# Performance work log

Measured on AMD Instinct MI355X. Metric: run time of the kernel, lower is better.

Reference implementation:

```python
import jax, jax.numpy as jnp
import numpy as np

N_HEAD = 16
N_KV_HEAD = 4
HEAD_DIM = 128
EPS = 1e-6


def apply_rotary_emb(x, cos, sin):
    # x: (B,T,H,hd); cos/sin: (1,T,1,hd//2)
    d = x.shape[3] // 2
    x1, x2 = x[..., :d], x[..., d:]
    y1 = x1 * cos + x2 * sin
    y2 = x1 * -sin + x2 * cos
    return jnp.concatenate([y1, y2], axis=3).astype(x.dtype)


def rmsnorm(x):
    # flax nnx.RMSNorm with use_scale=False: x * rsqrt(mean(x^2) + eps)
    ms = jnp.mean(jnp.square(x), axis=-1, keepdims=True)
    return (x * jax.lax.rsqrt(ms + EPS)).astype(x.dtype)


def setup_inputs() -> dict:
    key = jax.random.key(0)
    ks = jax.random.split(key, 7)
    B, T, C = 4, 2048, 2048
    s = 0.02
    return {
        "x": jax.random.normal(ks[0], (B, T, C), jnp.float32),
        "cos": jax.random.normal(ks[1], (1, T, 1, HEAD_DIM // 2), jnp.float32),
        "sin": jax.random.normal(ks[2], (1, T, 1, HEAD_DIM // 2), jnp.float32),
        "Wq": jax.random.normal(ks[3], (C, N_HEAD * HEAD_DIM), jnp.float32) * s,
        "Wk": jax.random.normal(ks[4], (C, N_KV_HEAD * HEAD_DIM), jnp.float32) * s,
        "Wv": jax.random.normal(ks[5], (C, N_KV_HEAD * HEAD_DIM), jnp.float32) * s,
        "Wo": jax.random.normal(ks[6], (C, C), jnp.float32) * s,
    }


def reference(x, cos, sin, Wq, Wk, Wv, Wo):
    B, T, C = x.shape
    q = (x @ Wq).reshape(B, T, N_HEAD, HEAD_DIM)
    k = (x @ Wk).reshape(B, T, N_KV_HEAD, HEAD_DIM)
    v = (x @ Wv).reshape(B, T, N_KV_HEAD, HEAD_DIM)
    q = rmsnorm(apply_rotary_emb(q, cos, sin))
    k = rmsnorm(apply_rotary_emb(k, cos, sin))
    # (B,H,T,hd)
    q = jnp.transpose(q, (0, 2, 1, 3))
    k = jnp.transpose(k, (0, 2, 1, 3))
    v = jnp.transpose(v, (0, 2, 1, 3))
    nrep = N_HEAD // N_KV_HEAD
    k = jnp.repeat(k, nrep, axis=1)
    v = jnp.repeat(v, nrep, axis=1)
    scale = 1.0 / jnp.sqrt(jnp.float32(HEAD_DIM))
    att = jnp.einsum('bhqd,bhkd->bhqk', q, k) * scale
    mask = jnp.tril(jnp.ones((T, T), dtype=bool))[None, None, :, :]
    att = jnp.where(mask, att, -jnp.inf)
    att = jax.nn.softmax(att, axis=-1)
    y = jnp.einsum('bhqk,bhkd->bhqd', att, v)
    y = jnp.transpose(y, (0, 2, 1, 3)).reshape(B, T, -1)
    return y @ Wo
```

## Files before the change

kernel.cpp:

```cpp
#include <hip/hip_runtime.h>
#include <hip/hip_bf16.h>

typedef __attribute__((ext_vector_type(8))) short short8;
typedef __attribute__((ext_vector_type(4))) float f32x4;

#define B_SZ 4
#define T_SEQ 2048
#define C_DIM 2048
#define NH 16
#define NKV 4
#define HD 128

#define MFMA16 __builtin_amdgcn_mfma_f32_16x16x32_bf16

__device__ __forceinline__ unsigned short f2bf(float f) {
  union { __hip_bfloat16 h; unsigned short u; } v;
  v.h = __float2bfloat16(f);
  return v.u;
}
__device__ __forceinline__ float bf2f(unsigned short u) {
  union { unsigned short u; __hip_bfloat16 h; } v;
  v.u = u;
  return __bfloat162float(v.h);
}

__device__ __forceinline__ void gload_lds16(const unsigned short* g, unsigned short* l) {
  __builtin_amdgcn_global_load_lds(
      (const __attribute__((address_space(1))) unsigned int*)g,
      (__attribute__((address_space(3))) unsigned int*)l, 16, 0, 0);
}

__global__ void cast_x(const float* __restrict__ x, unsigned short* __restrict__ xb, int n4) {
  int i = blockIdx.x * blockDim.x + threadIdx.x;
  if (i < n4) {
    float4 f = ((const float4*)x)[i];
    ushort4 u = make_ushort4(f2bf(f.x), f2bf(f.y), f2bf(f.z), f2bf(f.w));
    ((ushort4*)xb)[i] = u;
  }
}

__global__ void wtransAll(const float* __restrict__ Wq, const float* __restrict__ Wk,
                          const float* __restrict__ Wv, const float* __restrict__ Wo,
                          unsigned short* __restrict__ WqkvT, unsigned short* __restrict__ WoT) {
  __shared__ float tile[32][33];
  int y = blockIdx.y;
  const float* W;
  unsigned short* Wt;
  int N, n0;
  if (y < 64) { W = Wq; Wt = WqkvT; N = 2048; n0 = y * 32; }
  else if (y < 80) { W = Wk; Wt = WqkvT + (size_t)2048 * 2048; N = 512; n0 = (y - 64) * 32; }
  else if (y < 96) { W = Wv; Wt = WqkvT + (size_t)2560 * 2048; N = 512; n0 = (y - 80) * 32; }
  else { W = Wo; Wt = WoT; N = 2048; n0 = (y - 96) * 32; }
  int k0 = blockIdx.x * 32;
  int tx = threadIdx.x, ty = threadIdx.y;
#pragma unroll
  for (int i = 0; i < 4; i++)
    tile[ty + i * 8][tx] = W[(size_t)(k0 + ty + i * 8) * N + n0 + tx];
  __syncthreads();
#pragma unroll
  for (int i = 0; i < 4; i++)
    Wt[(size_t)(n0 + ty + i * 8) * 2048 + k0 + tx] = f2bf(tile[tx][ty + i * 8]);
}

__global__ void vtrans(const unsigned short* __restrict__ qkv, unsigned short* __restrict__ Vt) {
  __shared__ unsigned short tile[32][34];
  int t0 = blockIdx.x * 32, d0 = blockIdx.y * 32;
  int b = blockIdx.z >> 2, kvh = blockIdx.z & 3;
  int tx = threadIdx.x, ty = threadIdx.y;
#pragma unroll
  for (int i = 0; i < 4; i++)
    tile[ty + i * 8][tx] =
        qkv[(size_t)(b * T_SEQ + t0 + ty + i * 8) * 3072 + 2560 + kvh * HD + d0 + tx];
  __syncthreads();
#pragma unroll
  for (int i = 0; i < 4; i++)
    Vt[((size_t)(b * NKV + kvh) * HD + d0 + ty + i * 8) * T_SEQ + t0 + tx] = tile[tx][ty + i * 8];
}

template <typename OutT>
__global__ __launch_bounds__(512, 2) void gemm128(const unsigned short* __restrict__ A,
                                                  const unsigned short* __restrict__ Bt,
                                                  OutT* __restrict__ Cc, int N, int K, int GX) {
  __shared__ alignas(16) unsigned short lds[2][3][128 * 64];
  const int tid = threadIdx.x, lane = tid & 63, wid = tid >> 6;
  const int wave_m = wid >> 2, wave_n = wid & 3;
  const int r16 = lane & 15, q4 = lane >> 4;
  const int sw = r16 & 7;

  int nwg = gridDim.x, orig = blockIdx.x;
  int qq = nwg >> 3, rr = nwg & 7;
  int xcd = orig & 7, loc = orig >> 3;
  int wg = (xcd < rr ? xcd * (qq + 1) : rr * (qq + 1) + (xcd - rr) * qq) + loc;
  int bx = wg % GX, by = wg / GX;
  const size_t row0 = (size_t)bx * 128, col0 = (size_t)by * 256;

  const unsigned short* Ab = A + row0 * K;
  const unsigned short* Bb0 = Bt + col0 * K;
  const unsigned short* Bb1 = Bt + (col0 + 128) * K;

  const int srow = lane >> 3, spb = lane & 7;
  auto stage = [&](const unsigned short* base, int buf, int slot, int k0) {
#pragma unroll
    for (int j = 0; j < 2; ++j) {
      int cw = j * 8 + wid;
      int row = cw * 8 + srow;
      gload_lds16(base + (size_t)row * K + k0 + ((spb ^ srow) * 8), &lds[buf][slot][cw * 512]);
    }
  };

  f32x4 acc[4][4];
  f32x4 zero = {0.f, 0.f, 0.f, 0.f};
#pragma unroll
  for (int m = 0; m < 4; m++)
#pragma unroll
    for (int n = 0; n < 4; n++) acc[m][n] = zero;

  const int NT = K / 64;
  stage(Ab, 0, 0, 0);
  stage(Bb0, 0, 1, 0);
  stage(Bb1, 0, 2, 0);
  stage(Ab, 1, 0, 64);
  asm volatile("s_waitcnt vmcnt(2)" ::: "memory");
  __builtin_amdgcn_s_barrier();

  short8 af[4][2], b01[2][2], b23[2][2];
  const int bslot = 1 + (wave_n >> 1);
  const int bro = (wave_n & 1) * 64;

  int cur = 0;
#pragma unroll 1
  for (int t = 0; t < NT; ++t) {
    const unsigned short* Ah = &lds[cur][0][0];
    const unsigned short* Bh = &lds[cur][bslot][0];
    const int k1 = t * 64 + 64, k2 = t * 64 + 128;
#pragma unroll
    for (int mf = 0; mf < 4; mf++)
#pragma unroll
      for (int kk = 0; kk < 2; kk++)
        af[mf][kk] =
            *(const short8*)(Ah + (wave_m * 64 + mf * 16 + r16) * 64 + (((kk * 4 + q4) ^ sw) * 8));
#pragma unroll
    for (int nf = 0; nf < 2; nf++)
#pragma unroll
      for (int kk = 0; kk < 2; kk++)
        b01[nf][kk] =
            *(const short8*)(Bh + (bro + nf * 16 + r16) * 64 + (((kk * 4 + q4) ^ sw) * 8));
    if (t + 1 < NT) stage(Bb0, cur ^ 1, 1, k1);
    __builtin_amdgcn_s_barrier();
    asm volatile("s_waitcnt lgkmcnt(0)" ::: "memory");
    __builtin_amdgcn_s_setprio(1);
#pragma unroll
    for (int mf = 0; mf < 4; mf++)
#pragma unroll
      for (int nf = 0; nf < 2; nf++)
#pragma unroll
        for (int kk = 0; kk < 2; kk++)
          acc[mf][nf] = MFMA16(af[mf][kk], b01[nf][kk], acc[mf][nf], 0, 0, 0);
    __builtin_amdgcn_s_setprio(0);
    __builtin_amdgcn_s_barrier();
#pragma unroll
    for (int nf = 0; nf < 2; nf++)
#pragma unroll
      for (int kk = 0; kk < 2; kk++)
        b23[nf][kk] =
            *(const short8*)(Bh + (bro + (nf + 2) * 16 + r16) * 64 + (((kk * 4 + q4) ^ sw) * 8));
    if (t + 1 < NT) stage(Bb1, cur ^ 1, 2, k1);
    if (t + 2 < NT) stage(Ab, cur, 0, k2);
    __builtin_amdgcn_s_barrier();
    asm volatile("s_waitcnt lgkmcnt(0)" ::: "memory");
    __builtin_amdgcn_s_setprio(1);
#pragma unroll
    for (int mf = 0; mf < 4; mf++)
#pragma unroll
      for (int nf = 0; nf < 2; nf++)
#pragma unroll
        for (int kk = 0; kk < 2; kk++)
          acc[mf][nf + 2] = MFMA16(af[mf][kk], b23[nf][kk], acc[mf][nf + 2], 0, 0, 0);
    __builtin_amdgcn_s_setprio(0);
    if (t + 2 < NT)
      asm volatile("s_waitcnt vmcnt(2)" ::: "memory");
    else if (t + 1 < NT)
      asm volatile("s_waitcnt vmcnt(0)" ::: "memory");
    __builtin_amdgcn_s_barrier();
    cur ^= 1;
  }

#pragma unroll
  for (int mf = 0; mf < 4; mf++)
#pragma unroll
    for (int nf = 0; nf < 4; nf++) {
      size_t rbase = row0 + wave_m * 64 + mf * 16 + q4 * 4;
      size_t cc = col0 + wave_n * 64 + nf * 16 + r16;
#pragma unroll
      for (int jj = 0; jj < 4; jj++) {
        if constexpr (sizeof(OutT) == 2)
          Cc[(rbase + jj) * (size_t)N + cc] = f2bf(acc[mf][nf][jj]);
        else
          Cc[(rbase + jj) * (size_t)N + cc] = acc[mf][nf][jj];
      }
    }
}

template <typename OutT>
__global__ __launch_bounds__(512, 2) void gemm256(const unsigned short* __restrict__ A,
                                                  const unsigned short* __restrict__ Bt,
                                                  OutT* __restrict__ Cc, int N, int K, int GX) {
  __shared__ alignas(16) unsigned short lds[2][4][128 * 64];
  const int tid = threadIdx.x, lane = tid & 63, wid = tid >> 6;
  const int wave_m = wid >> 2, wave_n = wid & 3;
  const int r16 = lane & 15, q4 = lane >> 4;
  const int sw = r16 & 7;

  int nwg = gridDim.x, orig = blockIdx.x;
  int qq = nwg >> 3, rr = nwg & 7;
  int xcd = orig & 7, loc = orig >> 3;
  int wg = (xcd < rr ? xcd * (qq + 1) : rr * (qq + 1) + (xcd - rr) * qq) + loc;
  int bx = wg % GX, by = wg / GX;
  const size_t row0 = (size_t)bx * 256, col0 = (size_t)by * 256;

  const unsigned short* Ab0 = A + row0 * K;
  const unsigned short* Ab1 = A + (row0 + 128) * K;
  const unsigned short* Bb0 = Bt + col0 * K;
  const unsigned short* Bb1 = Bt + (col0 + 128) * K;

  const int srow = lane >> 3, spb = lane & 7;
  auto stage = [&](const unsigned short* base, int buf, int slot, int k0) {
#pragma unroll
    for (int j = 0; j < 2; ++j) {
      int cw = j * 8 + wid;
      int row = cw * 8 + srow;
      gload_lds16(base + (size_t)row * K + k0 + ((spb ^ srow) * 8), &lds[buf][slot][cw * 512]);
    }
  };

  f32x4 acc[8][4];
  f32x4 zero = {0.f, 0.f, 0.f, 0.f};
#pragma unroll
  for (int m = 0; m < 8; m++)
#pragma unroll
    for (int n = 0; n < 4; n++) acc[m][n] = zero;

  const int NT = K / 64;
  stage(Ab0, 0, 0, 0);
  stage(Ab1, 0, 1, 0);
  stage(Bb0, 0, 2, 0);
  stage(Bb1, 0, 3, 0);
  stage(Ab0, 1, 0, 64);
  stage(Ab1, 1, 1, 64);
  asm volatile("s_waitcnt vmcnt(4)" ::: "memory");
  __builtin_amdgcn_s_barrier();

  short8 af[4][2], b01[2][2], b23[2][2];
  const int bslot = 2 + (wave_n >> 1);
  const int bro = (wave_n & 1) * 64;

  int cur = 0;
#pragma unroll 1
  for (int t = 0; t < NT; ++t) {
    const unsigned short* Ah = &lds[cur][wave_m][0];
    const unsigned short* Bh = &lds[cur][bslot][0];
    const int k1 = t * 64 + 64, k2 = t * 64 + 128;
#pragma unroll
    for (int mf = 0; mf < 4; mf++)
#pragma unroll
      for (int kk = 0; kk < 2; kk++)
        af[mf][kk] = *(const short8*)(Ah + (mf * 16 + r16) * 64 + (((kk * 4 + q4) ^ sw) * 8));
#pragma unroll
    for (int nf = 0; nf < 2; nf++)
#pragma unroll
      for (int kk = 0; kk < 2; kk++)
        b01[nf][kk] =
            *(const short8*)(Bh + (bro + nf * 16 + r16) * 64 + (((kk * 4 + q4) ^ sw) * 8));
    if (t + 1 < NT) stage(Bb0, cur ^ 1, 2, k1);
    __builtin_amdgcn_s_barrier();
    asm volatile("s_waitcnt lgkmcnt(0)" ::: "memory");
    __builtin_amdgcn_s_setprio(1);
#pragma unroll
    for (int mf = 0; mf < 4; mf++)
#pragma unroll
      for (int nf = 0; nf < 2; nf++)
#pragma unroll
        for (int kk = 0; kk < 2; kk++)
          acc[mf][nf] = MFMA16(af[mf][kk], b01[nf][kk], acc[mf][nf], 0, 0, 0);
    __builtin_amdgcn_s_setprio(0);
    __builtin_amdgcn_s_barrier();
#pragma unroll
    for (int nf = 0; nf < 2; nf++)
#pragma unroll
      for (int kk = 0; kk < 2; kk++)
        b23[nf][kk] =
            *(const short8*)(Bh + (bro + (nf + 2) * 16 + r16) * 64 + (((kk * 4 + q4) ^ sw) * 8));
    if (t + 1 < NT) stage(Bb1, cur ^ 1, 3, k1);
    __builtin_amdgcn_s_barrier();
    asm volatile("s_waitcnt lgkmcnt(0)" ::: "memory");
    __builtin_amdgcn_s_setprio(1);
#pragma unroll
    for (int mf = 0; mf < 4; mf++)
#pragma unroll
      for (int nf = 0; nf < 2; nf++)
#pragma unroll
        for (int kk = 0; kk < 2; kk++)
          acc[mf][nf + 2] = MFMA16(af[mf][kk], b23[nf][kk], acc[mf][nf + 2], 0, 0, 0);
    __builtin_amdgcn_s_setprio(0);
    __builtin_amdgcn_s_barrier();
#pragma unroll
    for (int mf = 0; mf < 4; mf++)
#pragma unroll
      for (int kk = 0; kk < 2; kk++)
        af[mf][kk] =
            *(const short8*)(Ah + ((mf + 4) * 16 + r16) * 64 + (((kk * 4 + q4) ^ sw) * 8));
    __builtin_amdgcn_s_barrier();
    asm volatile("s_waitcnt lgkmcnt(0)" ::: "memory");
    __builtin_amdgcn_s_setprio(1);
#pragma unroll
    for (int mf = 0; mf < 4; mf++)
#pragma unroll
      for (int nf = 0; nf < 2; nf++)
#pragma unroll
        for (int kk = 0; kk < 2; kk++)
          acc[mf + 4][nf] = MFMA16(af[mf][kk], b01[nf][kk], acc[mf + 4][nf], 0, 0, 0);
    __builtin_amdgcn_s_setprio(0);
    __builtin_amdgcn_s_barrier();
    if (t + 2 < NT) {
      stage(Ab0, cur, 0, k2);
      stage(Ab1, cur, 1, k2);
    }
    __builtin_amdgcn_s_barrier();
    __builtin_amdgcn_s_setprio(1);
#pragma unroll
    for (int mf = 0; mf < 4; mf++)
#pragma unroll
      for (int nf = 0; nf < 2; nf++)
#pragma unroll
        for (int kk = 0; kk < 2; kk++)
          acc[mf + 4][nf + 2] = MFMA16(af[mf][kk], b23[nf][kk], acc[mf + 4][nf + 2], 0, 0, 0);
    __builtin_amdgcn_s_setprio(0);
    if (t + 1 < NT) {
      if (t + 2 < NT)
        asm volatile("s_waitcnt vmcnt(4)" ::: "memory");
      else
        asm volatile("s_waitcnt vmcnt(0)" ::: "memory");
    }
    __builtin_amdgcn_s_barrier();
    cur ^= 1;
  }

#pragma unroll
  for (int mf = 0; mf < 8; mf++)
#pragma unroll
    for (int nf = 0; nf < 4; nf++) {
      size_t rbase = row0 + wave_m * 128 + mf * 16 + q4 * 4;
      size_t cc = col0 + wave_n * 64 + nf * 16 + r16;
#pragma unroll
      for (int jj = 0; jj < 4; jj++) {
        if constexpr (sizeof(OutT) == 2)
          Cc[(rbase + jj) * (size_t)N + cc] = f2bf(acc[mf][nf][jj]);
        else
          Cc[(rbase + jj) * (size_t)N + cc] = acc[mf][nf][jj];
      }
    }
}

__global__ void ropeAll(const unsigned short* __restrict__ qkv, const float* __restrict__ cosp,
                        const float* __restrict__ sinp, unsigned short* __restrict__ Qb,
                        unsigned short* __restrict__ Kb) {
  int gid = blockIdx.x * 4 + (threadIdx.x >> 6);
  int lane = threadIdx.x & 63;
  int hh = gid % 20;
  int bt = gid / 20;
  int t = bt % T_SEQ, b = bt / T_SEQ;
  int colbase;
  unsigned short* dst;
  float outscale;
  if (hh < 16) {
    colbase = hh * HD;
    dst = Qb + ((size_t)(b * NH + hh) * T_SEQ + t) * HD;
    outscale = 0.08838834764831845f;
  } else {
    int h2 = hh - 16;
    colbase = 2048 + h2 * HD;
    dst = Kb + ((size_t)(b * NKV + h2) * T_SEQ + t) * HD;
    outscale = 1.0f;
  }
  const unsigned short* src = qkv + (size_t)(b * T_SEQ + t) * 3072 + colbase;
  float x1 = bf2f(src[lane]), x2 = bf2f(src[64 + lane]);
  float c = cosp[t * 64 + lane], s = sinp[t * 64 + lane];
  float y1 = x1 * c + x2 * s;
  float y2 = x2 * c - x1 * s;
  float ss = y1 * y1 + y2 * y2;
#pragma unroll
  for (int d = 1; d < 64; d <<= 1) ss += __shfl_xor(ss, d);
  float r = rsqrtf(ss * (1.f / 128.f) + 1e-6f) * outscale;
  dst[lane] = f2bf(y1 * r);
  dst[64 + lane] = f2bf(y2 * r);
}

__global__ __launch_bounds__(512, 2) void attn(const unsigned short* __restrict__ Qn,
                                               const unsigned short* __restrict__ Kn,
                                               const unsigned short* __restrict__ Vt,
                                               unsigned short* __restrict__ Y) {
  __shared__ alignas(16) unsigned short lK[2][64 * 128];
  __shared__ alignas(16) unsigned short lV[2][128 * 64];
  __shared__ alignas(16) unsigned short pl[8][16 * 32];

  int lin = blockIdx.x;
  int low3 = lin & 7, rest = lin >> 3;
  int chi = rest >> 6, idx = rest & 63;
  int c = (chi << 3) | low3;
  int b = c >> 2, kvh = c & 3;
  int h = kvh * 4 + (idx >> 4);
  int qt = 15 - (idx & 15);
  int Q0 = qt * 128;

  int lane = threadIdx.x & 63, w = threadIdx.x >> 6;
  const int r16 = lane & 15, q4 = lane >> 4;
  const unsigned short* Qp = Qn + ((size_t)(b * NH + h) * T_SEQ + Q0 + w * 16) * HD;
  const unsigned short* Kp = Kn + (size_t)(b * NKV + kvh) * T_SEQ * HD;
  const unsigned short* Vp = Vt + (size_t)(b * NKV + kvh) * HD * T_SEQ;

  short8 qf[4];
#pragma unroll
  for (int i = 0; i < 4; i++) qf[i] = *(const short8*)(Qp + r16 * HD + i * 32 + q4 * 8);

  f32x4 zero = {0.f, 0.f, 0.f, 0.f};
  f32x4 o[8];
  float mrow[4], Lp[4];
#pragma unroll
  for (int nb = 0; nb < 8; nb++) o[nb] = zero;
#pragma unroll
  for (int j = 0; j < 4; j++) { mrow[j] = -1e30f; Lp[j] = 0.f; }

  auto stageK = [&](int kv0, int buf) {
#pragma unroll
    for (int j = 0; j < 2; ++j) {
      int cw = w * 2 + j;
      int row = cw * 4 + (lane >> 4);
      int cb = lane & 15;
      gload_lds16(Kp + (size_t)(kv0 + row) * HD + ((cb ^ (row & 7)) * 8), &lK[buf][cw * 512]);
    }
  };
  auto stageV = [&](int kv0, int buf) {
#pragma unroll
    for (int j = 0; j < 2; ++j) {
      int cw = w * 2 + j;
      int row = cw * 8 + (lane >> 3);
      int db = lane & 7;
      gload_lds16(Vp + (size_t)row * T_SEQ + kv0 + ((db ^ (row & 7)) * 8), &lV[buf][cw * 512]);
    }
  };

  const int ntiles = 2 * qt + 2;
  const int ntw = (Q0 + w * 16 + 79) >> 6;

  stageK(0, 0);
  stageV(0, 0);
  __syncthreads();
  int cur = 0;

  for (int t = 0; t < ntiles; ++t) {
    int kv0 = t * 64;
    if (t + 1 < ntiles) { stageK(kv0 + 64, cur ^ 1); stageV(kv0 + 64, cur ^ 1); }
    if (t < ntw) {
      f32x4 s[4];
      __builtin_amdgcn_s_setprio(1);
#pragma unroll
      for (int nt = 0; nt < 4; nt++) {
        f32x4 a0 = zero;
        int krow = nt * 16 + r16;
#pragma unroll
        for (int i = 0; i < 4; i++) {
          short8 kf =
              *(const short8*)(&lK[cur][krow * 128 + ((q4 * 8 + i * 32) ^ ((krow & 7) << 3))]);
          a0 = __builtin_amdgcn_mfma_f32_16x16x32_bf16(qf[i], kf, a0, 0, 0, 0);
        }
        s[nt] = a0;
      }
      __builtin_amdgcn_s_setprio(0);
      if (kv0 + 63 > Q0 + w * 16) {
#pragma unroll
        for (int nt = 0; nt < 4; nt++)
#pragma unroll
          for (int j = 0; j < 4; j++) {
            int col = kv0 + nt * 16 + r16;
            int row = Q0 + w * 16 + q4 * 4 + j;
            if (col > row) s[nt][j] = -1e30f;
          }
      }
      float pm[4];
#pragma unroll
      for (int j = 0; j < 4; j++)
        pm[j] = fmaxf(fmaxf(s[0][j], s[1][j]), fmaxf(s[2][j], s[3][j]));
#pragma unroll
      for (int d = 1; d < 16; d <<= 1)
#pragma unroll
        for (int j = 0; j < 4; j++) pm[j] = fmaxf(pm[j], __shfl_xor(pm[j], d));
      float dmax = -1e30f;
#pragma unroll
      for (int j = 0; j < 4; j++) dmax = fmaxf(dmax, pm[j] - mrow[j]);
      if (!__all(dmax <= 8.0f)) {
#pragma unroll
        for (int j = 0; j < 4; j++) {
          float mn = fmaxf(mrow[j], pm[j]);
          float al = __expf(mrow[j] - mn);
          mrow[j] = mn;
          Lp[j] *= al;
#pragma unroll
          for (int nb = 0; nb < 8; nb++) o[nb][j] *= al;
        }
      }
#pragma unroll
      for (int nt = 0; nt < 4; nt++)
#pragma unroll
        for (int j = 0; j < 4; j++) {
          float p = __expf(s[nt][j] - mrow[j]);
          Lp[j] += p;
          s[nt][j] = p;
        }
#pragma unroll
      for (int ks = 0; ks < 2; ks++) {
#pragma unroll
        for (int nn = 0; nn < 2; nn++)
#pragma unroll
          for (int j = 0; j < 4; j++) {
            int prow = q4 * 4 + j;
            int col = nn * 16 + r16;
            pl[w][prow * 32 + (col ^ (q4 << 3))] = f2bf(s[ks * 2 + nn][j]);
          }
        int t0 = q4 * 8;
        int sw0 = ((r16 >> 2) & 3) << 3;
        short8 pf0 = *(const short8*)(&pl[w][r16 * 32 + (t0 ^ sw0)]);
        __builtin_amdgcn_s_setprio(1);
#pragma unroll
        for (int nb = 0; nb < 8; nb++) {
          int vrow = nb * 16 + r16;
          short8 vf =
              *(const short8*)(&lV[cur][vrow * 64 + ((ks * 32 + q4 * 8) ^ ((vrow & 7) << 3))]);
          o[nb] = __builtin_amdgcn_mfma_f32_16x16x32_bf16(pf0, vf, o[nb], 0, 0, 0);
        }
        __builtin_amdgcn_s_setprio(0);
      }
    }
    __syncthreads();
    cur ^= 1;
  }

  float linv[4];
#pragma unroll
  for (int j = 0; j < 4; j++) {
    float v = Lp[j];
#pragma unroll
    for (int d = 1; d < 16; d <<= 1) v += __shfl_xor(v, d);
    linv[j] = 1.f / v;
  }
#pragma unroll
  for (int nb = 0; nb < 8; nb++)
#pragma unroll
    for (int j = 0; j < 4; j++) {
      size_t row = (size_t)Q0 + w * 16 + q4 * 4 + j;
      Y[((size_t)(b * T_SEQ) + row) * (NH * HD) + h * HD + nb * 16 + r16] =
          f2bf(o[nb][j] * linv[j]);
    }
}

extern "C" void kernel_launch(void* const* d_in, const int* in_sizes, int n_in,
                              void* d_out, int out_size, void* d_ws, size_t ws_size,
                              hipStream_t stream) {
  const float* x = (const float*)d_in[0];
  const float* cosp = (const float*)d_in[1];
  const float* sinp = (const float*)d_in[2];
  const float* Wq = (const float*)d_in[3];
  const float* Wk = (const float*)d_in[4];
  const float* Wv = (const float*)d_in[5];
  const float* Wo = (const float*)d_in[6];
  float* out = (float*)d_out;

  char* ws = (char*)d_ws;
  size_t off = 0;
  auto alloc = [&](size_t bytes) { void* p = ws + off; off += bytes; return p; };
  const size_t BT = (size_t)B_SZ * T_SEQ;
  unsigned short* xb = (unsigned short*)alloc(BT * C_DIM * 2);
  unsigned short* WqkvT = (unsigned short*)alloc((size_t)3072 * 2048 * 2);
  unsigned short* WoT = (unsigned short*)alloc((size_t)2048 * 2048 * 2);
  unsigned short* qkv = (unsigned short*)alloc(BT * 3072 * 2);
  unsigned short* Kb = (unsigned short*)alloc(BT * 512 * 2);
  unsigned short* Vb = (unsigned short*)alloc(BT * 512 * 2);
  unsigned short* Qb = xb;
  unsigned short* Yb = qkv;

  dim3 tb(32, 8);
  cast_x<<<16384, 256, 0, stream>>>(x, xb, (int)(BT * C_DIM / 4));
  wtransAll<<<dim3(64, 160), tb, 0, stream>>>(Wq, Wk, Wv, Wo, WqkvT, WoT);

  gemm128<unsigned short><<<768, 512, 0, stream>>>(xb, WqkvT, qkv, 3072, 2048, 64);

  ropeAll<<<(B_SZ * T_SEQ * 20) / 4, 256, 0, stream>>>(qkv, cosp, sinp, Qb, Kb);
  vtrans<<<dim3(64, 4, 16), tb, 0, stream>>>(qkv, Vb);

  attn<<<dim3(1024), 512, 0, stream>>>(Qb, Kb, Vb, Yb);

  gemm256<float><<<256, 512, 0, stream>>>(Yb, WoT, out, 2048, 2048, 32);
}
```

Measured before the change: 428.0 us.

## Rewrite attention with 32x32 MFMA, transposed S, and register-only P exchange

The attention kernel moves from 16x16x32 to 32x32x16 bf16 MFMA. Each wave now owns 32 query rows and the block shrinks to 4 waves of 256 threads. S is computed transposed, so each lane holds one query row's scores and the row max and sum need only one cross-half shuffle instead of a 16-lane reduction. The P operand is rebuilt from registers with xor-32 shuffles rather than an LDS round-trip, and outputs are stored as ushort4. This trades more registers per wave and fewer waves per block for less LDS traffic and fewer reductions.

```diff
diff --git a/kernel.cpp b/kernel.cpp
--- a/kernel.cpp
+++ b/kernel.cpp
@@ -3,6 +3,7 @@
 
 typedef __attribute__((ext_vector_type(8))) short short8;
 typedef __attribute__((ext_vector_type(4))) float f32x4;
+typedef __attribute__((ext_vector_type(16))) float f32x16;
 
 #define B_SZ 4
 #define T_SEQ 2048
@@ -12,6 +13,7 @@
 #define HD 128
 
 #define MFMA16 __builtin_amdgcn_mfma_f32_16x16x32_bf16
+#define MFMA32 __builtin_amdgcn_mfma_f32_32x32x16_bf16
 
 __device__ __forceinline__ unsigned short f2bf(float f) {
   union { __hip_bfloat16 h; unsigned short u; } v;
@@ -22,6 +24,9 @@
   union { unsigned short u; __hip_bfloat16 h; } v;
   v.u = u;
   return __bfloat162float(v.h);
+}
+__device__ __forceinline__ unsigned pkbf(float lo, float hi) {
+  return (unsigned)f2bf(lo) | ((unsigned)f2bf(hi) << 16);
 }
 
 __device__ __forceinline__ void gload_lds16(const unsigned short* g, unsigned short* l) {
@@ -395,13 +400,12 @@
   dst[64 + lane] = f2bf(y2 * r);
 }
 
-__global__ __launch_bounds__(512, 2) void attn(const unsigned short* __restrict__ Qn,
+__global__ __launch_bounds__(256, 2) void attn(const unsigned short* __restrict__ Qn,
                                                const unsigned short* __restrict__ Kn,
                                                const unsigned short* __restrict__ Vt,
                                                unsigned short* __restrict__ Y) {
   __shared__ alignas(16) unsigned short lK[2][64 * 128];
   __shared__ alignas(16) unsigned short lV[2][128 * 64];
-  __shared__ alignas(16) unsigned short pl[8][16 * 32];
 
   int lin = blockIdx.x;
   int low3 = lin & 7, rest = lin >> 3;
@@ -413,27 +417,27 @@
   int Q0 = qt * 128;
 
   int lane = threadIdx.x & 63, w = threadIdx.x >> 6;
-  const int r16 = lane & 15, q4 = lane >> 4;
-  const unsigned short* Qp = Qn + ((size_t)(b * NH + h) * T_SEQ + Q0 + w * 16) * HD;
+  const int q5 = lane & 31, hi = lane >> 5, l7 = lane & 7;
+  const int qrow = Q0 + w * 32 + q5;
+  const unsigned short* Qp = Qn + ((size_t)(b * NH + h) * T_SEQ + qrow) * HD;
   const unsigned short* Kp = Kn + (size_t)(b * NKV + kvh) * T_SEQ * HD;
   const unsigned short* Vp = Vt + (size_t)(b * NKV + kvh) * HD * T_SEQ;
 
-  short8 qf[4];
-#pragma unroll
-  for (int i = 0; i < 4; i++) qf[i] = *(const short8*)(Qp + r16 * HD + i * 32 + q4 * 8);
-
-  f32x4 zero = {0.f, 0.f, 0.f, 0.f};
-  f32x4 o[8];
-  float mrow[4], Lp[4];
-#pragma unroll
-  for (int nb = 0; nb < 8; nb++) o[nb] = zero;
-#pragma unroll
-  for (int j = 0; j < 4; j++) { mrow[j] = -1e30f; Lp[j] = 0.f; }
+  short8 qf[8];
+#pragma unroll
+  for (int i = 0; i < 8; i++) qf[i] = *(const short8*)(Qp + i * 16 + hi * 8);
+
+  f32x16 o4[4];
+#pragma unroll
+  for (int d = 0; d < 4; d++)
+#pragma unroll
+    for (int r = 0; r < 16; r++) o4[d][r] = 0.f;
+  float mrow = -1e30f, Lp = 0.f;
 
   auto stageK = [&](int kv0, int buf) {
 #pragma unroll
-    for (int j = 0; j < 2; ++j) {
-      int cw = w * 2 + j;
+    for (int j = 0; j < 4; ++j) {
+      int cw = w * 4 + j;
       int row = cw * 4 + (lane >> 4);
       int cb = lane & 15;
       gload_lds16(Kp + (size_t)(kv0 + row) * HD + ((cb ^ (row & 7)) * 8), &lK[buf][cw * 512]);
@@ -441,8 +445,8 @@
   };
   auto stageV = [&](int kv0, int buf) {
 #pragma unroll
-    for (int j = 0; j < 2; ++j) {
-      int cw = w * 2 + j;
+    for (int j = 0; j < 4; ++j) {
+      int cw = w * 4 + j;
       int row = cw * 8 + (lane >> 3);
       int db = lane & 7;
       gload_lds16(Vp + (size_t)row * T_SEQ + kv0 + ((db ^ (row & 7)) * 8), &lV[buf][cw * 512]);
@@ -450,7 +454,7 @@
   };
 
   const int ntiles = 2 * qt + 2;
-  const int ntw = (Q0 + w * 16 + 79) >> 6;
+  const int ntw = (Q0 + w * 32 + 95) >> 6;
 
   stageK(0, 0);
   stageV(0, 0);
@@ -461,104 +465,86 @@
     int kv0 = t * 64;
     if (t + 1 < ntiles) { stageK(kv0 + 64, cur ^ 1); stageV(kv0 + 64, cur ^ 1); }
     if (t < ntw) {
-      f32x4 s[4];
-      __builtin_amdgcn_s_setprio(1);
-#pragma unroll
-      for (int nt = 0; nt < 4; nt++) {
-        f32x4 a0 = zero;
-        int krow = nt * 16 + r16;
-#pragma unroll
-        for (int i = 0; i < 4; i++) {
-          short8 kf =
-              *(const short8*)(&lK[cur][krow * 128 + ((q4 * 8 + i * 32) ^ ((krow & 7) << 3))]);
-          a0 = __builtin_amdgcn_mfma_f32_16x16x32_bf16(qf[i], kf, a0, 0, 0, 0);
-        }
-        s[nt] = a0;
-      }
-      __builtin_amdgcn_s_setprio(0);
-      if (kv0 + 63 > Q0 + w * 16) {
-#pragma unroll
-        for (int nt = 0; nt < 4; nt++)
-#pragma unroll
-          for (int j = 0; j < 4; j++) {
-            int col = kv0 + nt * 16 + r16;
-            int row = Q0 + w * 16 + q4 * 4 + j;
-            if (col > row) s[nt][j] = -1e30f;
-          }
-      }
-      float pm[4];
-#pragma unroll
-      for (int j = 0; j < 4; j++)
-        pm[j] = fmaxf(fmaxf(s[0][j], s[1][j]), fmaxf(s[2][j], s[3][j]));
-#pragma unroll
-      for (int d = 1; d < 16; d <<= 1)
-#pragma unroll
-        for (int j = 0; j < 4; j++) pm[j] = fmaxf(pm[j], __shfl_xor(pm[j], d));
-      float dmax = -1e30f;
-#pragma unroll
-      for (int j = 0; j < 4; j++) dmax = fmaxf(dmax, pm[j] - mrow[j]);
-      if (!__all(dmax <= 8.0f)) {
-#pragma unroll
-        for (int j = 0; j < 4; j++) {
-          float mn = fmaxf(mrow[j], pm[j]);
-          float al = __expf(mrow[j] - mn);
-          mrow[j] = mn;
-          Lp[j] *= al;
-#pragma unroll
-          for (int nb = 0; nb < 8; nb++) o[nb][j] *= al;
-        }
-      }
-#pragma unroll
-      for (int nt = 0; nt < 4; nt++)
-#pragma unroll
-        for (int j = 0; j < 4; j++) {
-          float p = __expf(s[nt][j] - mrow[j]);
-          Lp[j] += p;
-          s[nt][j] = p;
-        }
-#pragma unroll
-      for (int ks = 0; ks < 2; ks++) {
-#pragma unroll
-        for (int nn = 0; nn < 2; nn++)
-#pragma unroll
-          for (int j = 0; j < 4; j++) {
-            int prow = q4 * 4 + j;
-            int col = nn * 16 + r16;
-            pl[w][prow * 32 + (col ^ (q4 << 3))] = f2bf(s[ks * 2 + nn][j]);
-          }
-        int t0 = q4 * 8;
-        int sw0 = ((r16 >> 2) & 3) << 3;
-        short8 pf0 = *(const short8*)(&pl[w][r16 * 32 + (t0 ^ sw0)]);
+#pragma unroll
+      for (int kt = 0; kt < 2; kt++) {
+        f32x16 st;
+#pragma unroll
+        for (int r = 0; r < 16; r++) st[r] = 0.f;
+        const int krow = kt * 32 + q5;
         __builtin_amdgcn_s_setprio(1);
 #pragma unroll
-        for (int nb = 0; nb < 8; nb++) {
-          int vrow = nb * 16 + r16;
-          short8 vf =
-              *(const short8*)(&lV[cur][vrow * 64 + ((ks * 32 + q4 * 8) ^ ((vrow & 7) << 3))]);
-          o[nb] = __builtin_amdgcn_mfma_f32_16x16x32_bf16(pf0, vf, o[nb], 0, 0, 0);
+        for (int i = 0; i < 8; i++) {
+          short8 kf = *(const short8*)(&lK[cur][krow * 128 + (((2 * i + hi) ^ l7) * 8)]);
+          st = MFMA32(kf, qf[i], st, 0, 0, 0);
         }
         __builtin_amdgcn_s_setprio(0);
+        if (kv0 + kt * 32 + 31 > Q0 + w * 32) {
+#pragma unroll
+          for (int r = 0; r < 16; r++) {
+            int kg = kv0 + kt * 32 + (r & 3) + 8 * (r >> 2) + 4 * hi;
+            if (kg > qrow) st[r] = -1e30f;
+          }
+        }
+        float pm = st[0];
+#pragma unroll
+        for (int r = 1; r < 16; r++) pm = fmaxf(pm, st[r]);
+        pm = fmaxf(pm, __shfl_xor(pm, 32));
+        if (!__all(pm - mrow <= 8.0f)) {
+          float mn = fmaxf(mrow, pm);
+          float al = __expf(mrow - mn);
+          mrow = mn;
+          Lp *= al;
+#pragma unroll
+          for (int d = 0; d < 4; d++)
+#pragma unroll
+            for (int r = 0; r < 16; r++) o4[d][r] *= al;
+        }
+        float p[16];
+#pragma unroll
+        for (int r = 0; r < 16; r++) {
+          p[r] = __expf(st[r] - mrow);
+          Lp += p[r];
+        }
+#pragma unroll
+        for (int ks = 0; ks < 2; ks++) {
+          unsigned x0 = pkbf(p[8 * ks + 0], p[8 * ks + 1]);
+          unsigned x1 = pkbf(p[8 * ks + 2], p[8 * ks + 3]);
+          unsigned y0 = pkbf(p[8 * ks + 4], p[8 * ks + 5]);
+          unsigned y1 = pkbf(p[8 * ks + 6], p[8 * ks + 7]);
+          unsigned sx0 = __shfl_xor((int)x0, 32), sx1 = __shfl_xor((int)x1, 32);
+          unsigned sy0 = __shfl_xor((int)y0, 32), sy1 = __shfl_xor((int)y1, 32);
+          union { unsigned u[4]; short8 s; } pw;
+          pw.u[0] = hi ? sy0 : x0;
+          pw.u[1] = hi ? sy1 : x1;
+          pw.u[2] = hi ? y0 : sx0;
+          pw.u[3] = hi ? y1 : sx1;
+          const int cb = 4 * kt + 2 * ks + hi;
+          __builtin_amdgcn_s_setprio(1);
+#pragma unroll
+          for (int db = 0; db < 4; db++) {
+            int vrow = db * 32 + q5;
+            short8 vf = *(const short8*)(&lV[cur][vrow * 64 + ((cb ^ l7) * 8)]);
+            o4[db] = MFMA32(vf, pw.s, o4[db], 0, 0, 0);
+          }
+          __builtin_amdgcn_s_setprio(0);
+        }
       }
     }
     __syncthreads();
     cur ^= 1;
   }
 
-  float linv[4];
-#pragma unroll
-  for (int j = 0; j < 4; j++) {
-    float v = Lp[j];
-#pragma unroll
-    for (int d = 1; d < 16; d <<= 1) v += __shfl_xor(v, d);
-    linv[j] = 1.f / v;
-  }
-#pragma unroll
-  for (int nb = 0; nb < 8; nb++)
-#pragma unroll
-    for (int j = 0; j < 4; j++) {
-      size_t row = (size_t)Q0 + w * 16 + q4 * 4 + j;
-      Y[((size_t)(b * T_SEQ) + row) * (NH * HD) + h * HD + nb * 16 + r16] =
-          f2bf(o[nb][j] * linv[j]);
+  float L = Lp + __shfl_xor(Lp, 32);
+  float linv = 1.f / L;
+  unsigned short* Yp = Y + ((size_t)(b * T_SEQ) + qrow) * (NH * HD) + h * HD;
+#pragma unroll
+  for (int db = 0; db < 4; db++)
+#pragma unroll
+    for (int g = 0; g < 4; g++) {
+      int d0 = db * 32 + g * 8 + 4 * hi;
+      ushort4 v = make_ushort4(f2bf(o4[db][g * 4 + 0] * linv), f2bf(o4[db][g * 4 + 1] * linv),
+                               f2bf(o4[db][g * 4 + 2] * linv), f2bf(o4[db][g * 4 + 3] * linv));
+      *(ushort4*)(Yp + d0) = v;
     }
 }
 
@@ -596,7 +582,7 @@
   ropeAll<<<(B_SZ * T_SEQ * 20) / 4, 256, 0, stream>>>(qkv, cosp, sinp, Qb, Kb);
   vtrans<<<dim3(64, 4, 16), tb, 0, stream>>>(qkv, Vb);
 
-  attn<<<dim3(1024), 512, 0, stream>>>(Qb, Kb, Vb, Yb);
+  attn<<<dim3(1024), 256, 0, stream>>>(Qb, Kb, Vb, Yb);
 
   gemm256<float><<<256, 512, 0, stream>>>(Yb, WoT, out, 2048, 2048, 32);
 }
```

Measured after the change: 395.9 us. -7.5%, faster.
